# Kernel tuning notes

Hardware: AMD Instinct MI355X
Metric: run time of the kernel (lower is better)

Reference implementation:

```python
import jax, jax.numpy as jnp
import numpy as np
import random as _pyrandom

# static config (must match init_kwargs)
LAYER_NODES = 2
NUM_LEVELS = 2
KERNEL = 3
STRIDE = 2
DILATION = 3
BN_EPS = 1e-5
B, T, C = 64, 4096, 64

# ---- static interleave-index builders (replace torch per-element cat loops with one gather) ----

def _joint_indices(a_len, b_len, node_idx):
    # Block.joint: interleave a (cur) with skip=2**(node_idx-1) elems of b (prev) per a-step.
    skip = 2 ** (node_idx - 1)
    idx, cnt = [], 0
    for i in range(a_len):
        for _ in range(skip):
            if cnt >= b_len:
                break
            idx.append(a_len + cnt)
            cnt += 1
        idx.append(i)
    return np.asarray(idx, np.int32)


def _joint_explict_indices(a_len, b_len, c_len):
    # Block.joint_explict: round-robin a,b,c then tails in order a,b,c.
    m = min(a_len, b_len, c_len)
    idx = []
    for t in range(m):
        idx += [t, a_len + t, a_len + b_len + t]
    idx += list(range(m, a_len))
    idx += list(range(a_len + m, a_len + b_len))
    idx += list(range(a_len + b_len + m, a_len + b_len + c_len))
    return np.asarray(idx, np.int32)


def _dpadding_indices(a_len, num_padding):
    # Block.dpadding: duplicate every skip_cnt-th element until num_padding extras inserted.
    if num_padding == 0:
        return np.arange(a_len, dtype=np.int32)
    target = a_len + num_padding
    skip_cnt = a_len // num_padding
    mult = None
    if skip_cnt == 0:
        mult = num_padding // a_len
        skip_cnt = 1
    entries = []  # list-of-lists mimics torch list entries (slab counts as 1 entry, as in source)
    rem = num_padding
    for i in range(a_len):
        if rem == 0:
            entries.append(list(range(i, a_len)))
            break
        if i % skip_cnt == 0:
            entries.append([i])
            rem -= 1
        if mult is not None:
            entries.extend([[i]] * mult)
        entries.append([i])
    if len(entries) > target:  # randrange pop path; deterministic seed (never hit for these shapes)
        rng = _pyrandom.Random(0)
        for _ in range(len(entries) - target):
            entries.pop(rng.randrange(len(entries)))
    return np.asarray([k for e in entries for k in e], np.int32)


def _sew_up_indices(a_len, b_len, cur_layer, sp, st):
    # Block.sew_up for cur_layer > 0; st carries the mutable skip_* counters.
    idx = []
    cnt_a = cnt_b = 0
    while cnt_a < a_len:
        if sp:
            break
        if cnt_a == 0:
            pv = cnt_b  # prev_val captured once in torch source
            for _ in range(st['skip_p']):
                idx.append(a_len + pv)
                cnt_b += 1
            if cur_layer % 2 != 0:
                idx.append(0)
                cnt_a += 1
            if cnt_a == 0:
                cnt_a = 1
            continue
        for _ in range(st['skip_n']):
            if cnt_b >= b_len:
                break
            idx.append(a_len + cnt_b)
            cnt_b += 1
        if not st['skip_t']:
            for _ in range(st['skip_s']):
                if cnt_b >= b_len:
                    break
                idx.append(a_len + cnt_b)
                cnt_b += 1
                st['skip_t'] = True
        else:
            for _j in range(st['skip_d']):
                for _i in range(st['skip_s']):
                    if cnt_b >= b_len:
                        break
                    idx.append(a_len + cnt_b)
                    cnt_b += 1
                if cnt_a >= a_len:
                    break
                idx.append(cnt_a)
                cnt_a += 1
                st['skip_t'] = False
            continue
        idx.append(cnt_a)
        cnt_a += 1
    idx += [a_len + j for j in range(cnt_b, b_len)]
    if sp:
        idx += list(range(cnt_a, a_len))
    st['skip_s'] += 1
    st['skip_n'] = 3 * st['skip_n'] + st['skip_s'] + st['skip_d'] * st['skip_s']
    if cur_layer % 2 != 0:
        st['skip_p'] += 1
    return np.asarray(idx, np.int32)

# ---- jax compute blocks ----

def _conv_block(y, v, g, b):
    # weight_norm(Conv1d): w = g * v / ||v||_(in,k) per out-channel; then MaxPool1d(3,2,pad=1), ELU (dropout=0)
    nrm = jnp.sqrt(jnp.sum(v * v, axis=(1, 2), keepdims=True))
    w = (g[:, None, None] / nrm) * v
    y = jax.lax.conv_general_dilated(y, w, (STRIDE,), 'VALID', rhs_dilation=(DILATION,),
                                     dimension_numbers=('NCH', 'OIH', 'NCH'))
    y = y + b[None, :, None]
    y = jax.lax.reduce_window(y, -jnp.inf, jax.lax.max, (1, 1, KERNEL), (1, 1, STRIDE),
                              ((0, 0), (0, 0), (1, 1)))
    return jax.nn.elu(y)


def _batchnorm(y, gamma, beta):
    # BatchNorm1d training-mode batch stats (biased var), per channel over (N, L)
    mu = jnp.mean(y, axis=(0, 2), keepdims=True)
    var = jnp.mean((y - mu) ** 2, axis=(0, 2), keepdims=True)
    return gamma[None, :, None] * (y - mu) * jax.lax.rsqrt(var + BN_EPS) + beta[None, :, None]


def _communicate(xn, prev_out, node_idx, mean, std, conv_v, conv_g, conv_b, bn_gamma, bn_beta):
    if node_idx == 0:
        return xn
    while prev_out.shape[2] != xn.shape[2]:  # static-shape loop
        prev_out = jnp.diff(prev_out, axis=2)
    out_mean = 0.8 * xn / mean + 0.2 * prev_out
    out_std = 0.8 * xn / std + 0.2 * prev_out
    L = xn.shape[2]
    je = _joint_explict_indices(L, L, L)
    joined = jnp.concatenate([out_mean, prev_out, out_std], axis=2)[:, :, je]
    y = jnp.exp(_conv_block(joined, conv_v, conv_g, conv_b) ** 2 / -2)
    pad_idx = _dpadding_indices(y.shape[2], L - y.shape[2])
    y = y[:, :, pad_idx]
    y = _batchnorm(y, bn_gamma, bn_beta)
    y = jax.nn.elu(y)  # Dropout(0.1) in eval -> identity
    return xn + y


def _forward(x, conv_v, conv_g, conv_b, bn_gamma, bn_beta):
    x = jnp.transpose(x, (0, 2, 1))  # [B, C, T]
    mean = jnp.mean(x)
    std = jnp.std(x, ddof=1)  # torch.std is unbiased
    # Graph.build_graph: level l node (l*LAYER_NODES + i) = x strided by LAYER_NODES, l+1 times
    nodes = {}
    for i in range(LAYER_NODES):
        cur = x
        for lvl in range(NUM_LEVELS):
            cur = cur[:, :, i::LAYER_NODES]
            assert cur.shape[2] >= 10, 'sp stat-padding path not exercised with these shapes'
            nodes[lvl * LAYER_NODES + i] = cur
    st = dict(skip_p=1, skip_s=1, skip_d=2, skip_n=3, skip_t=False)
    prev_layer_out = None
    cur_layer_out = None
    for i in range(NUM_LEVELS):
        cur_layer_out = None
        prev_out = None
        for j in range(LAYER_NODES + 1):
            cur_node = i * LAYER_NODES if j == LAYER_NODES else j + i * LAYER_NODES
            node_idx = j % LAYER_NODES
            out = _communicate(nodes[cur_node], prev_out, node_idx, mean, std,
                               conv_v, conv_g, conv_b, bn_gamma, bn_beta)
            prev_out = out
            if cur_layer_out is None:
                cur_layer_out = out
            if node_idx != 0:
                ji = _joint_indices(prev_out.shape[2], cur_layer_out.shape[2], node_idx)
                cur_layer_out = jnp.concatenate([prev_out, cur_layer_out], axis=2)[:, :, ji]
            if j == LAYER_NODES and i > 0:  # sew_up is identity at level 0
                si = _sew_up_indices(cur_layer_out.shape[2], prev_layer_out.shape[2], i, False, st)
                cur_layer_out = jnp.concatenate([cur_layer_out, prev_layer_out], axis=2)[:, :, si]
        prev_layer_out = cur_layer_out
    return cur_layer_out  # [B, C, 6144]


def setup_inputs() -> dict:
    key = jax.random.key(0)
    k1, k2, k3 = jax.random.split(key, 3)
    return {
        'x': jax.random.normal(k1, (B, T, C), dtype=jnp.float32),
        'conv_v': jax.random.normal(k2, (C, C, KERNEL), dtype=jnp.float32) * 0.1,
        'conv_g': jax.random.uniform(k3, (C,), dtype=jnp.float32) + 0.5,
        'conv_b': jnp.zeros((C,), jnp.float32),
        'bn_gamma': jnp.ones((C,), jnp.float32),
        'bn_beta': jnp.zeros((C,), jnp.float32),
    }


def reference(x, conv_v, conv_g, conv_b, bn_gamma, bn_beta):
    return _forward(x, conv_v, conv_g, conv_b, bn_gamma, bn_beta)
```

## Files before the change

kernel.cpp:

```cpp
#include <hip/hip_runtime.h>
#include <math.h>

#define BB 64
#define TT 4096
#define CC 64

constexpr int L0v = 2048, U0v = 3069, V0v = 1535, P0v = 2048;
constexpr int L1v = 1024, U1v = 1533, V1v = 767,  P1v = 1024;
constexpr int OUTL = 6144;
constexpr long NTOT = (long)BB * TT * CC;
#define VB 30
#define NB0 52
#define NB1 26
#define NTILE ((NB0 + NB1) * 64)
#define SRTOT 87
#define GSTR 89
#define RSTR 65
#define EROWS 63

__global__ __launch_bounds__(256) void transpose_stats(const float* __restrict__ x,
                                                       float* __restrict__ xtr,
                                                       double* __restrict__ part) {
  __shared__ float tile[64][65];
  __shared__ double sred[8];
  const int tt = blockIdx.x;
  const int b = blockIdx.y;
  const int t0 = tt * 64;
  const long xbase = (long)b * TT * CC + (long)t0 * CC;
  const int tid = threadIdx.x;
  double a = 0, q = 0;
  {
    const int c4 = (tid & 15) * 4;
    const int r0 = tid >> 4;
#pragma unroll
    for (int rr = 0; rr < 4; rr++) {
      int r = r0 + rr * 16;
      float4 v = *(const float4*)&x[xbase + r * 64 + c4];
      tile[r][c4] = v.x; tile[r][c4 + 1] = v.y;
      tile[r][c4 + 2] = v.z; tile[r][c4 + 3] = v.w;
      a += (double)v.x + (double)v.y + (double)v.z + (double)v.w;
      q += (double)v.x * v.x + (double)v.y * v.y + (double)v.z * v.z + (double)v.w * v.w;
    }
  }
  __syncthreads();
  {
    const int t4 = (tid & 15) * 4;
    const int c0 = tid >> 4;
#pragma unroll
    for (int cc = 0; cc < 4; cc++) {
      int c = c0 + cc * 16;
      float4 v;
      v.x = tile[t4][c]; v.y = tile[t4 + 1][c];
      v.z = tile[t4 + 2][c]; v.w = tile[t4 + 3][c];
      *(float4*)&xtr[((long)(b * 64 + c)) * TT + t0 + t4] = v;
    }
  }
  for (int off = 32; off > 0; off >>= 1) {
    a += __shfl_down(a, off);
    q += __shfl_down(q, off);
  }
  if ((tid & 63) == 0) { sred[(tid >> 6) * 2] = a; sred[(tid >> 6) * 2 + 1] = q; }
  __syncthreads();
  if (tid == 0) {
    part[(b * 64 + tt) * 2]     = sred[0] + sred[2] + sred[4] + sred[6];
    part[(b * 64 + tt) * 2 + 1] = sred[1] + sred[3] + sred[5] + sred[7];
  }
}

__device__ __host__ inline int pad_idx(int p, int brk, int dup, int sub) {
  if (p < brk) { int q = p / 3; int r = p - 3 * q; return 2 * q + (r == 2 ? 1 : 0); }
  if (p < brk + 2) return dup;
  return p - sub;
}

__device__ inline int fmap_code(int k) {
  if (k == 0) return 2048 + 0;
  if (k == 1) return 0;
  if (k < 5462) {
    int m = k - 2;
    int c = m / 12;
    int j = m - 12 * c;
    if (j <= 3)  return 2048 + (1 + 9 * c + j);
    if (j == 4)  return 1 + 3 * c;
    if (j <= 8)  return 2048 + (9 * c + j);
    if (j == 9)  return 2 + 3 * c;
    if (j == 10) return 2048 + (9 + 9 * c);
    return 3 + 3 * c;
  }
  return k - 4096;
}

__global__ __launch_bounds__(256) void prep(const double* __restrict__ part,
                                            double* __restrict__ stats,
                                            const float* __restrict__ v,
                                            const float* __restrict__ g,
                                            float* __restrict__ wt,
                                            int* __restrict__ codes) {
  const int blk = blockIdx.x;
  const int tid = threadIdx.x;
  if (blk == 0) {
    __shared__ double s1[256], s2[256];
    double a = 0, q = 0;
    for (int i = tid; i < 4096; i += 256) { a += part[2 * i]; q += part[2 * i + 1]; }
    s1[tid] = a; s2[tid] = q;
    __syncthreads();
    for (int s = 128; s > 0; s >>= 1) {
      if (tid < s) { s1[tid] += s1[tid + s]; s2[tid] += s2[tid + s]; }
      __syncthreads();
    }
    if (tid == 0) {
      double n = (double)NTOT;
      double mean = s1[0] / n;
      double var = (s2[0] - s1[0] * s1[0] / n) / (n - 1.0);
      stats[0] = mean; stats[1] = sqrt(var);
      stats[2] = 0.8 / mean;
      stats[3] = 0.8 / sqrt(var);
    }
  } else if (blk <= 64) {
    int o = blk - 1;
    __shared__ float red[256];
    __shared__ float scale;
    float vv = (tid < 192) ? v[o * 192 + tid] : 0.f;
    red[tid] = vv * vv;
    __syncthreads();
    for (int s = 128; s > 0; s >>= 1) {
      if (tid < s) red[tid] += red[tid + s];
      __syncthreads();
    }
    if (tid == 0) scale = g[o] / sqrtf(red[0]);
    __syncthreads();
    if (tid < 192) {
      int i = tid / 3, k = tid - 3 * i;
      wt[(k * 64 + i) * 64 + o] = scale * vv;
    }
  } else {
    int k = (blk - 65) * 256 + tid;
    if (k < OUTL) {
      int s = fmap_code(k);
      int type, xi, yi = 0;
      if (s < 2048) {
        if ((s & 1) == 0) { type = 0; xi = 2 * s; }
        else { int p = s >> 1; yi = pad_idx(p, 768, 512, 257); xi = 4 * p + 3; type = 2; }
      } else {
        int p = s - 2048;
        if ((p & 1) == 0) { type = 0; xi = p; }
        else { int q = p >> 1; yi = pad_idx(q, 1536, 1024, 513); xi = 2 * q + 1; type = 1; }
      }
      codes[k] = type | (xi << 2) | (yi << 14);
    }
  }
}

__global__ __launch_bounds__(256, 7) void conv_pool(
    const float* __restrict__ x, const float* __restrict__ wt,
    const float* __restrict__ cbias, const double* __restrict__ stats,
    float* __restrict__ y10, float* __restrict__ y11,
    float* __restrict__ part) {
  const int b = blockIdx.x;
  const int jb = blockIdx.y;
  const bool lev0 = jb < NB0;
  const int v0 = (lev0 ? jb : jb - NB0) * VB;
  const int L = lev0 ? L0v : L1v;
  const int U = lev0 ? U0v : U1v;
  const int V = lev0 ? V0v : V1v;
  const int mult = lev0 ? 2 : 4;
  const int off1 = lev0 ? 1 : 3;
  const int mid = lev0 ? 1024 : 512;
  float* __restrict__ y1 = lev0 ? y10 : y11;

  const int tid = threadIdx.x;
  const int lane = tid & 63;
  const int og = __builtin_amdgcn_readfirstlane((tid >> 6) * 16);

  const int a0 = (v0 == 0) ? 0 : (2 * v0 - 1) / 3;

  __shared__ __align__(16) float4 S2[16 * GSTR];
  float* cbf = (float*)S2;
  float* red = (float*)S2 + 4096;

  const float ivm = (float)stats[2];
  const float ivs = (float)stats[3];
  const long xbase = (long)b * TT * CC;

  for (int idx = tid; idx < SRTOT * 16; idx += 256) {
    int d = idx >> 4, g = idx & 15;
    int T = (d < 44) ? (2 * a0 + d) : (2 * a0 + d - 44);
    int Tc = min(max(T, 0), L - 1);
    long row = (long)(mult * Tc) * CC + ((d < 44) ? 0 : off1) * CC;
    S2[g * GSTR + d] = *(const float4*)&x[xbase + row + g * 4];
  }
  __syncthreads();

  const int rho = (lane <= 41) ? lane : ((lane == 63) ? 0 : (44 + 2 * (lane - 42)));

  float acc[16];
#pragma unroll
  for (int oo = 0; oo < 16; oo++) acc[oo] = 0.f;

  for (int k = 0; k < 3; k++) {
    const float4* Sk = S2 + rho + k;
    const float* wk = wt + k * 4096 + og;
#pragma unroll 4
    for (int i4 = 0; i4 < 16; i4++) {
      float4 xv = Sk[i4 * GSTR];
      const float* wp = wk + i4 * 256;
#pragma unroll
      for (int oo = 0; oo < 16; oo++) {
        float w0 = wp[oo], w1 = wp[64 + oo], w2 = wp[128 + oo], w3 = wp[192 + oo];
        acc[oo] = fmaf(xv.x, w0, acc[oo]);
        acc[oo] = fmaf(xv.y, w1, acc[oo]);
        acc[oo] = fmaf(xv.z, w2, acc[oo]);
        acc[oo] = fmaf(xv.w, w3, acc[oo]);
      }
    }
  }

  __syncthreads();
  if (lane < EROWS) {
#pragma unroll
    for (int oo = 0; oo < 16; oo++)
      cbf[lane * RSTR + og + oo] = acc[oo];
  }
  __syncthreads();

  const int o = tid >> 2;
  const float bias = cbias[o];
  float a1 = 0.f, a2 = 0.f;
  for (int vq = tid & 3; vq < VB; vq += 4) {
    int v = v0 + vq;
    if (v < V) {
      float m3 = -INFINITY;
#pragma unroll
      for (int p = 0; p < 3; p++) {
        int u = 2 * v - 1 + p;
        float mv = -INFINITY;
        if (u >= 0 && u < U) {
          int a = u / 3;
          int r = u - 3 * a;
          int ai = a - a0;
          if (r == 2) {
            mv = cbf[(2 * ai + 1) * RSTR + o] + bias;
          } else {
            float e1 = cbf[(42 + ai) * RSTR + o];
            float e0 = cbf[(2 * ai) * RSTR + o];
            mv = fmaf(r ? ivs : ivm, e1, fmaf(0.2f, e0, bias));
          }
        }
        m3 = fmaxf(m3, mv);
      }
      float e = (m3 > 0.f) ? m3 : (expf(m3) - 1.f);
      float y = expf(-0.5f * e * e);
      y1[(long)(b * 64 + o) * V + v] = y;
      float wv = (v < mid) ? (float)(2 - (v & 1)) : ((v == mid) ? 2.f : 1.f);
      a1 += wv * y;
      a2 += wv * y * y;
    }
  }
  red[o * 4 + (tid & 3)] = a1;
  red[256 + o * 4 + (tid & 3)] = a2;
  __syncthreads();
  if (tid < 64) {
    float s1 = red[tid * 4] + red[tid * 4 + 1] + red[tid * 4 + 2] + red[tid * 4 + 3];
    float s2 = red[256 + tid * 4] + red[256 + tid * 4 + 1] + red[256 + tid * 4 + 2] + red[256 + tid * 4 + 3];
    long tile = (long)jb * 64 + b;
    part[tile * 128 + tid * 2] = s1;
    part[tile * 128 + tid * 2 + 1] = s2;
  }
}

__global__ __launch_bounds__(256) void bn_reduce(const float* __restrict__ part,
                                                 const float* __restrict__ gamma,
                                                 const float* __restrict__ beta,
                                                 float* __restrict__ cf0,
                                                 float* __restrict__ cf1) {
  const int bc = blockIdx.x;
  const int lev = bc >> 6, c = bc & 63;
  const long t_lo = lev ? (long)NB0 * 64 : 0;
  const long t_hi = lev ? (long)(NB0 + NB1) * 64 : (long)NB0 * 64;
  const int tid = threadIdx.x;
  double a = 0, q = 0;
  for (long t = t_lo + tid; t < t_hi; t += 256) {
    a += part[t * 128 + c * 2];
    q += part[t * 128 + c * 2 + 1];
  }
  __shared__ double s1[256], s2[256];
  s1[tid] = a; s2[tid] = q;
  __syncthreads();
  for (int s = 128; s > 0; s >>= 1) {
    if (tid < s) { s1[tid] += s1[tid + s]; s2[tid] += s2[tid + s]; }
    __syncthreads();
  }
  if (tid == 0) {
    double n = (double)BB * (lev ? P1v : P0v);
    double mu = s1[0] / n;
    double var = s2[0] / n - mu * mu;
    float rsig = 1.0f / sqrtf((float)var + 1e-5f);
    float A = gamma[c] * rsig;
    float Bv = beta[c] - (float)mu * A;
    float* cf = lev ? cf1 : cf0;
    cf[2 * c] = A;
    cf[2 * c + 1] = Bv;
  }
}

__global__ __launch_bounds__(256) void final_fused(
    const float* __restrict__ xtr, const float* __restrict__ y10,
    const float* __restrict__ y11, const float* __restrict__ cf0,
    const float* __restrict__ cf1, const int* __restrict__ codes,
    float* __restrict__ out) {
  const int bc = blockIdx.x;
  const int c = bc & 63;
  const int tid = threadIdx.x;
  __shared__ float xs[4096];
  __shared__ float y0s[1536];
  __shared__ float y1s[768];

  const float* xr = xtr + (long)bc * TT;
  for (int i = tid; i < 1024; i += 256)
    *(float4*)&xs[i * 4] = *(const float4*)&xr[i * 4];
  const float* y0r = y10 + (long)bc * V0v;
  for (int i = tid; i < 384; i += 256) {
    if (i < 383) *(float4*)&y0s[i * 4] = *(const float4*)&y0r[i * 4];
    else { y0s[1532] = y0r[1532]; y0s[1533] = y0r[1533]; y0s[1534] = y0r[1534]; }
  }
  const float* y1r = y11 + (long)bc * V1v;
  for (int i = tid; i < 192; i += 256) {
    if (i < 191) *(float4*)&y1s[i * 4] = *(const float4*)&y1r[i * 4];
    else { y1s[764] = y1r[764]; y1s[765] = y1r[765]; y1s[766] = y1r[766]; }
  }
  __syncthreads();

  const float A0 = cf0[2 * c], B0 = cf0[2 * c + 1];
  const float A1 = cf1[2 * c], B1 = cf1[2 * c + 1];
  float* orow = out + (long)bc * OUTL;
#pragma unroll 4
  for (int i = 0; i < 24; i++) {
    int k = i * 256 + tid;
    int code = codes[k];
    int type = code & 3;
    int xi = (code >> 2) & 4095;
    int yi = code >> 14;
    float xv = xs[xi];
    float yv = (type == 2) ? y1s[yi] : y0s[yi];
    float A = (type == 0) ? 0.f : ((type == 2) ? A1 : A0);
    float Bv = (type == 0) ? 0.f : ((type == 2) ? B1 : B0);
    float z = fmaf(A, yv, Bv);
    float e = (z > 0.f) ? z : (expf(z) - 1.f);
    orow[k] = xv + e;
  }
}

extern "C" void kernel_launch(void* const* d_in, const int* in_sizes, int n_in,
                              void* d_out, int out_size, void* d_ws, size_t ws_size,
                              hipStream_t stream) {
  const float* x   = (const float*)d_in[0];
  const float* cv  = (const float*)d_in[1];
  const float* cg  = (const float*)d_in[2];
  const float* cb  = (const float*)d_in[3];
  const float* gam = (const float*)d_in[4];
  const float* bet = (const float*)d_in[5];
  float* out = (float*)d_out;

  char* ws = (char*)d_ws;
  size_t cur = 0;
  auto alloc = [&](size_t bytes) -> char* {
    char* p = ws + cur;
    cur = (cur + bytes + 255) & ~(size_t)255;
    return p;
  };
  double* part   = (double*)alloc(4096 * 2 * sizeof(double));
  double* stats  = (double*)alloc(4 * sizeof(double));
  float*  wt     = (float*)alloc(3 * 64 * 64 * sizeof(float));
  float*  bnp    = (float*)alloc((size_t)NTILE * 128 * sizeof(float));
  float*  cf0    = (float*)alloc(128 * sizeof(float));
  float*  cf1    = (float*)alloc(128 * sizeof(float));
  int*    codes  = (int*)alloc(OUTL * sizeof(int));
  float*  xtr    = (float*)alloc((size_t)BB * CC * TT * sizeof(float));
  float*  y10    = (float*)alloc((size_t)4096 * V0v * sizeof(float));
  float*  y11    = (float*)alloc((size_t)4096 * V1v * sizeof(float));

  transpose_stats<<<dim3(64, 64), 256, 0, stream>>>(x, xtr, part);
  prep<<<89, 256, 0, stream>>>(part, stats, cv, cg, wt, codes);

  conv_pool<<<dim3(64, NB0 + NB1), 256, 0, stream>>>(x, wt, cb, stats, y10, y11, bnp);

  bn_reduce<<<128, 256, 0, stream>>>(bnp, gam, bet, cf0, cf1);

  final_fused<<<4096, 256, 0, stream>>>(xtr, y10, y11, cf0, cf1, codes, out);
}
```

Baseline: 316.9 us.

## Compute conv in conv_pool with bf16x3 split MFMA instead of FP32 FMAs

The conv inner product in conv_pool is moved from scalar FP32 FMA loops to 16x16x32 bf16 MFMA instructions. Both activations and weights are split into three bf16 parts (high, mid, low), and six cross-product MFMAs are issued to keep close to FP32 accuracy. Weights are pre-split and re-laid out in prep, and the activations are split while being staged into shared memory. Launch bounds drop from 7 to 4 waves per SIMD to allow more registers, and the weight fragments are read directly from global memory.

```diff
diff --git a/kernel.cpp b/kernel.cpp
--- a/kernel.cpp
+++ b/kernel.cpp
@@ -14,9 +14,25 @@
 #define NB1 26
 #define NTILE ((NB0 + NB1) * 64)
 #define SRTOT 87
-#define GSTR 89
+#define XSTR 72
+#define XPL  (SRTOT * XSTR)
 #define RSTR 65
 #define EROWS 63
+
+using short8  = __attribute__((ext_vector_type(8))) short;
+using floatx4 = __attribute__((ext_vector_type(4))) float;
+
+__device__ inline unsigned bf16rn(float f) {
+  unsigned u = __float_as_uint(f);
+  return (u + 0x7fffu + ((u >> 16) & 1u)) >> 16;
+}
+__device__ inline void bf16split3(float x, unsigned short& h, unsigned short& m,
+                                  unsigned short& l) {
+  unsigned uh = bf16rn(x); h = (unsigned short)uh;
+  float r1 = x - __uint_as_float(uh << 16);
+  unsigned um = bf16rn(r1); m = (unsigned short)um;
+  l = (unsigned short)bf16rn(r1 - __uint_as_float(um << 16));
+}
 
 __global__ __launch_bounds__(256) void transpose_stats(const float* __restrict__ x,
                                                        float* __restrict__ xtr,
@@ -94,7 +110,9 @@
                                             double* __restrict__ stats,
                                             const float* __restrict__ v,
                                             const float* __restrict__ g,
-                                            float* __restrict__ wt,
+                                            unsigned short* __restrict__ wth,
+                                            unsigned short* __restrict__ wtm,
+                                            unsigned short* __restrict__ wtl,
                                             int* __restrict__ codes) {
   const int blk = blockIdx.x;
   const int tid = threadIdx.x;
@@ -131,7 +149,11 @@
     __syncthreads();
     if (tid < 192) {
       int i = tid / 3, k = tid - 3 * i;
-      wt[(k * 64 + i) * 64 + o] = scale * vv;
+      float w = scale * vv;
+      unsigned short h, m, l;
+      bf16split3(w, h, m, l);
+      int kk = o * 192 + k * 64 + i;
+      wth[kk] = h; wtm[kk] = m; wtl[kk] = l;
     }
   } else {
     int k = (blk - 65) * 256 + tid;
@@ -151,8 +173,11 @@
   }
 }
 
-__global__ __launch_bounds__(256, 7) void conv_pool(
-    const float* __restrict__ x, const float* __restrict__ wt,
+__global__ __launch_bounds__(256, 4) void conv_pool(
+    const float* __restrict__ x,
+    const unsigned short* __restrict__ wth,
+    const unsigned short* __restrict__ wtm,
+    const unsigned short* __restrict__ wtl,
     const float* __restrict__ cbias, const double* __restrict__ stats,
     float* __restrict__ y10, float* __restrict__ y11,
     float* __restrict__ part) {
@@ -170,13 +195,13 @@
 
   const int tid = threadIdx.x;
   const int lane = tid & 63;
-  const int og = __builtin_amdgcn_readfirstlane((tid >> 6) * 16);
+  const int w = tid >> 6;
 
   const int a0 = (v0 == 0) ? 0 : (2 * v0 - 1) / 3;
 
-  __shared__ __align__(16) float4 S2[16 * GSTR];
-  float* cbf = (float*)S2;
-  float* red = (float*)S2 + 4096;
+  __shared__ __align__(16) unsigned short Xs[3 * XPL];
+  float* cbf = (float*)Xs;
+  float* red = (float*)Xs + 4096;
 
   const float ivm = (float)stats[2];
   const float ivs = (float)stats[3];
@@ -187,39 +212,60 @@
     int T = (d < 44) ? (2 * a0 + d) : (2 * a0 + d - 44);
     int Tc = min(max(T, 0), L - 1);
     long row = (long)(mult * Tc) * CC + ((d < 44) ? 0 : off1) * CC;
-    S2[g * GSTR + d] = *(const float4*)&x[xbase + row + g * 4];
-  }
-  __syncthreads();
-
-  const int rho = (lane <= 41) ? lane : ((lane == 63) ? 0 : (44 + 2 * (lane - 42)));
-
-  float acc[16];
-#pragma unroll
-  for (int oo = 0; oo < 16; oo++) acc[oo] = 0.f;
-
-  for (int k = 0; k < 3; k++) {
-    const float4* Sk = S2 + rho + k;
-    const float* wk = wt + k * 4096 + og;
-#pragma unroll 4
-    for (int i4 = 0; i4 < 16; i4++) {
-      float4 xv = Sk[i4 * GSTR];
-      const float* wp = wk + i4 * 256;
-#pragma unroll
-      for (int oo = 0; oo < 16; oo++) {
-        float w0 = wp[oo], w1 = wp[64 + oo], w2 = wp[128 + oo], w3 = wp[192 + oo];
-        acc[oo] = fmaf(xv.x, w0, acc[oo]);
-        acc[oo] = fmaf(xv.y, w1, acc[oo]);
-        acc[oo] = fmaf(xv.z, w2, acc[oo]);
-        acc[oo] = fmaf(xv.w, w3, acc[oo]);
-      }
-    }
-  }
-
-  __syncthreads();
-  if (lane < EROWS) {
-#pragma unroll
-    for (int oo = 0; oo < 16; oo++)
-      cbf[lane * RSTR + og + oo] = acc[oo];
+    float4 vr = *(const float4*)&x[xbase + row + g * 4];
+    ushort4 hv, mv, lv;
+    bf16split3(vr.x, hv.x, mv.x, lv.x);
+    bf16split3(vr.y, hv.y, mv.y, lv.y);
+    bf16split3(vr.z, hv.z, mv.z, lv.z);
+    bf16split3(vr.w, hv.w, mv.w, lv.w);
+    int off = d * XSTR + g * 4;
+    *(ushort4*)&Xs[off]           = hv;
+    *(ushort4*)&Xs[XPL + off]     = mv;
+    *(ushort4*)&Xs[2 * XPL + off] = lv;
+  }
+  __syncthreads();
+
+  const int r16 = lane & 15;
+  const int hgrp = lane >> 4;
+  const int row = 16 * w + r16;
+  const int rho = (row <= 41) ? row : ((row == 63) ? 0 : (2 * row - 40));
+
+  floatx4 acc[4];
+#pragma unroll
+  for (int n = 0; n < 4; n++) acc[n] = floatx4{0.f, 0.f, 0.f, 0.f};
+
+#pragma unroll 1
+  for (int s = 0; s < 6; s++) {
+    const int tap = s >> 1, chb = (s & 1) * 32;
+    const int offA = (rho + tap) * XSTR + chb + hgrp * 8;
+    short8 ah = *(const short8*)&Xs[offA];
+    short8 am = *(const short8*)&Xs[XPL + offA];
+    short8 al = *(const short8*)&Xs[2 * XPL + offA];
+    const int offB = r16 * 192 + s * 32 + hgrp * 8;
+#pragma unroll
+    for (int n = 0; n < 4; n++) {
+      const int ob = offB + n * 16 * 192;
+      short8 bh = *(const short8*)&wth[ob];
+      short8 bm = *(const short8*)&wtm[ob];
+      short8 bl = *(const short8*)&wtl[ob];
+      acc[n] = __builtin_amdgcn_mfma_f32_16x16x32_bf16(ah, bh, acc[n], 0, 0, 0);
+      acc[n] = __builtin_amdgcn_mfma_f32_16x16x32_bf16(ah, bm, acc[n], 0, 0, 0);
+      acc[n] = __builtin_amdgcn_mfma_f32_16x16x32_bf16(am, bh, acc[n], 0, 0, 0);
+      acc[n] = __builtin_amdgcn_mfma_f32_16x16x32_bf16(ah, bl, acc[n], 0, 0, 0);
+      acc[n] = __builtin_amdgcn_mfma_f32_16x16x32_bf16(al, bh, acc[n], 0, 0, 0);
+      acc[n] = __builtin_amdgcn_mfma_f32_16x16x32_bf16(am, bm, acc[n], 0, 0, 0);
+    }
+  }
+
+  __syncthreads();
+#pragma unroll
+  for (int n = 0; n < 4; n++) {
+#pragma unroll
+    for (int r = 0; r < 4; r++) {
+      int er = 16 * w + 4 * hgrp + r;
+      if (er < EROWS)
+        cbf[er * RSTR + n * 16 + r16] = acc[n][r];
+    }
   }
   __syncthreads();
 
@@ -370,7 +416,9 @@
   };
   double* part   = (double*)alloc(4096 * 2 * sizeof(double));
   double* stats  = (double*)alloc(4 * sizeof(double));
-  float*  wt     = (float*)alloc(3 * 64 * 64 * sizeof(float));
+  unsigned short* wth = (unsigned short*)alloc(64 * 192 * sizeof(unsigned short));
+  unsigned short* wtm = (unsigned short*)alloc(64 * 192 * sizeof(unsigned short));
+  unsigned short* wtl = (unsigned short*)alloc(64 * 192 * sizeof(unsigned short));
   float*  bnp    = (float*)alloc((size_t)NTILE * 128 * sizeof(float));
   float*  cf0    = (float*)alloc(128 * sizeof(float));
   float*  cf1    = (float*)alloc(128 * sizeof(float));
@@ -380,9 +428,10 @@
   float*  y11    = (float*)alloc((size_t)4096 * V1v * sizeof(float));
 
   transpose_stats<<<dim3(64, 64), 256, 0, stream>>>(x, xtr, part);
-  prep<<<89, 256, 0, stream>>>(part, stats, cv, cg, wt, codes);
-
-  conv_pool<<<dim3(64, NB0 + NB1), 256, 0, stream>>>(x, wt, cb, stats, y10, y11, bnp);
+  prep<<<89, 256, 0, stream>>>(part, stats, cv, cg, wth, wtm, wtl, codes);
+
+  conv_pool<<<dim3(64, NB0 + NB1), 256, 0, stream>>>(
+      x, wth, wtm, wtl, cb, stats, y10, y11, bnp);
 
   bn_reduce<<<128, 256, 0, stream>>>(bnp, gam, bet, cf0, cf1);
 
```

After: 390.3 us. 23.1% more time.
